# Performance work log

Measured on AMD Instinct MI355X. Metric: run time of the kernel, lower is better.

The kernel has to match this reference:

```python
import jax, jax.numpy as jnp
import numpy as np
import math

NP2 = 64      # number of RF pulses
V = 32768     # number of voxels


def _shift_matrix(kmax):
    """EPG shift matrix, exact translation of EPG_shift_matrices."""
    N = 3 * (kmax + 1)
    S = np.zeros(N * N, dtype=np.complex64)
    kidx = list(range(3, N, 3)); sidx = [x - 3 for x in kidx]
    S[[a + N * b for a, b in zip(kidx, sidx)]] = 1
    kidx = list(range(4, N, 3)); kidx.pop(); sidx = [x + 3 for x in kidx]
    S[[a + N * b for a, b in zip(kidx, sidx)]] = 1
    kidx = list(range(2, N, 3))
    S[[a + N * b for a, b in zip(kidx, kidx)]] = 1
    S = S.reshape(N, N).T.copy()
    S[0:2, 4] = 1
    return jnp.asarray(S, dtype=jnp.complex64)


def _rf_rot_all(theta):
    """RF rotation matrices for all pulses at once. theta: [P] complex -> [P,3,3]."""
    a = jnp.abs(theta)
    phi = jnp.angle(theta)
    ca2 = (jnp.cos(a / 2) ** 2).astype(jnp.complex64)
    sa2 = jnp.sin(a / 2) ** 2
    sa = jnp.sin(a)
    ca = jnp.cos(a).astype(jnp.complex64)
    ep = jnp.exp(1j * phi)
    em = jnp.exp(-1j * phi)
    e2m = jnp.exp(-2j * phi)
    r00 = ca2
    r10 = e2m * sa2
    r20 = -0.5j * em * sa
    r01 = jnp.conj(r10)
    r11 = ca2
    r21 = 0.5j * ep * sa
    r02 = -1j * ep * sa
    r12 = 1j * em * sa
    r22 = ca
    row0 = jnp.stack([r00, r01, r02], axis=-1)
    row1 = jnp.stack([r10, r11, r12], axis=-1)
    row2 = jnp.stack([r20, r21, r22], axis=-1)
    return jnp.stack([row0, row1, row2], axis=-2).astype(jnp.complex64)


def _epg_gre_f0(theta, T1, T2, TR):
    """Single-compartment GRE EPG recurrence. Returns F0 signal [V, np2].

    Uses full-width (kmax) state updates every pulse: states beyond
    kmax_per_pulse are exactly zero on the ramp-up and cannot influence
    F0 on the ramp-down, so F0 matches the variable-width torch loop.
    """
    np2 = theta.shape[0]
    kmax = np2 - 1
    kpp_max = math.ceil(np2 / 2)
    if kpp_max < kmax:
        kmax = kpp_max
    K = kmax + 1
    N = 3 * K
    v = T1.shape[0]

    St = _shift_matrix(kmax).T                      # [N,N], so S @ f == f @ St
    E1 = jnp.exp(-TR / T1)[:, 0]                    # [V]
    E2 = jnp.exp(-TR / T2)[:, 0]                    # [V]
    # diagonal of kron(I_K, diag(E2,E2,E1)) per voxel -> [V,N]
    e = jnp.tile(jnp.stack([E2, E2, E1], axis=1), (1, K)).astype(jnp.complex64)
    b = jnp.zeros((v, N), jnp.complex64).at[:, 2].set((1 - E1).astype(jnp.complex64))

    A_all = _rf_rot_all(theta)                      # [np2,3,3]
    FF0 = jnp.zeros((v, N), jnp.complex64).at[:, 2].set(1.0)

    def step(FF, A):
        # block-diag kron(I_K, A) applied to the state vector
        Fcol = jnp.einsum('ab,vkb->vka', A, FF.reshape(v, K, 3)).reshape(v, N)
        # relaxation * shift + recovery
        FFn = e * (Fcol @ St) + b
        FFn = FFn.at[:, 0].set(jnp.conj(FFn[:, 0]))
        return FFn, Fcol[:, 0]

    _, F0 = jax.lax.scan(step, FF0, A_all)          # F0: [np2, V]
    return F0.T                                     # [V, np2]


def setup_inputs() -> dict:
    key = jax.random.key(0)
    k1, k2, k3, k4, k5 = jax.random.split(key, 5)
    flip = jax.random.uniform(k1, (NP2,), minval=0.1, maxval=math.pi / 2)
    phase = jax.random.uniform(k2, (NP2,), minval=-math.pi, maxval=math.pi)
    theta_re = (flip * jnp.cos(phase)).astype(jnp.float32)
    theta_im = (flip * jnp.sin(phase)).astype(jnp.float32)
    PD = jax.random.uniform(k3, (V, 1), minval=0.2, maxval=1.0)
    T1 = jax.random.uniform(k4, (V, 1), minval=300.0, maxval=1500.0)
    T2 = jax.random.uniform(k5, (V, 1), minval=20.0, maxval=120.0)
    qmaps = jnp.stack([PD, T1, T2], axis=0).astype(jnp.float32)  # [3,V,1]
    TR = jnp.array([10.0], jnp.float32)
    return {"theta_re": theta_re, "theta_im": theta_im, "TR": TR,
            "quantitative_maps": qmaps}


def reference(theta_re, theta_im, TR, quantitative_maps):
    theta = (theta_re + 1j * theta_im).astype(jnp.complex64)
    PD = quantitative_maps[0]   # [V,1]
    T1 = quantitative_maps[1]   # [V,1]
    T2 = quantitative_maps[2]   # [V,1]
    s = _epg_gre_f0(theta, T1, T2, TR)   # [V, np2] complex
    return jnp.abs(s) * PD
```

## Files before the change

### kernel.cpp

```cpp
#include <hip/hip_runtime.h>
#include <hip/hip_fp16.h>
#include <math.h>


#define NP2 64
#define ROR1  0x121
#define ROR15 0x12F
#define RSHL1 0x101

__device__ __forceinline__ unsigned h2u(__half2 x) {
    unsigned u; __builtin_memcpy(&u, &x, 4); return u;
}
__device__ __forceinline__ __half2 u2h(unsigned u) {
    __half2 h; __builtin_memcpy(&h, &u, 4); return h;
}
template<int CTRL>
__device__ __forceinline__ __half2 rroth(__half2 x) {
    return u2h((unsigned)__builtin_amdgcn_mov_dpp((int)h2u(x), CTRL, 0xF, 0xF, true));
}

__global__ void coef_kernel(const float* __restrict__ theta_re,
                            const float* __restrict__ theta_im,
                            unsigned* __restrict__ cw)
{
    const int t = threadIdx.x;
    if (t < NP2) {
        const float tre = theta_re[t], tim = theta_im[t];
        const float a2 = tre * tre + tim * tim;
        const float inva = __frsqrt_rn(a2);
        const float a = a2 * inva;
        const float c = tre * inva, s = tim * inva;
        float cp = 1.f, sp = 0.f;
        if (t > 0) {
            const float ure = theta_re[t - 1], uim = theta_im[t - 1];
            const float ia = __frsqrt_rn(ure * ure + uim * uim);
            cp = ure * ia; sp = uim * ia;
        }
        const float cd = cp * c + sp * s;
        const float sd = sp * c - cp * s;
        float sa, ca;
        __sincosf(a, &sa, &ca);
        const float ca2 = 0.5f + 0.5f * ca;
        const float sa2 = 0.5f - 0.5f * ca;
        unsigned* row = cw + t * 8;
        const float vals[8] = { cd, sd, ca2, sa2, sa, ca, 0.5f * sa, 0.f };
        for (int j = 0; j < 8; ++j) {
            const __half h = __float2half(vals[j]);
            __half2 hp = __halves2half2(h, h);
            unsigned u; __builtin_memcpy(&u, &hp, 4);
            row[j] = u;
        }
    } else if (t < NP2 + 8) {
        cw[NP2 * 8 + (t - NP2)] = 0u;
    }
}

__device__ __forceinline__ void slot_mat(
    __half2 Pr, __half2 Pi, __half2 Mr, __half2 Mi, __half2& Zr, __half2& Zi,
    __half2 ec, __half2 es, __half2 esn,
    __half2 ca2, __half2 sa2, __half2 sa, __half2 ca, __half2 hh,
    __half2 pE1, __half2 rec,
    __half2& nPr, __half2& nPi, __half2& nMr, __half2& nMi)
{
    const __half2 hPr = __hfma2(ec, Pr, __hmul2(esn, Pi));
    const __half2 hPi = __hfma2(ec, Pi, __hmul2(es,  Pr));
    const __half2 hMr = __hfma2(ec, Mr, __hmul2(es,  Mi));
    const __half2 hMi = __hfma2(ec, Mi, __hmul2(esn, Mr));
    const __half2 ezr = __hfma2(pE1, Zr, rec);
    const __half2 ezi = __hmul2(pE1, Zi);
    const __half2 szr = __hmul2(sa, ezr);
    const __half2 szi = __hmul2(sa, ezi);
    const __half2 szrn = __hneg2(szr);
    const __half2 szin = __hneg2(szi);
    nPr = __hfma2(ca2, hPr, __hfma2(sa2, hMr, szi));
    nPi = __hfma2(ca2, hPi, __hfma2(sa2, hMi, szrn));
    nMr = __hfma2(sa2, hPr, __hfma2(ca2, hMr, szin));
    nMi = __hfma2(sa2, hPi, __hfma2(ca2, hMi, szr));
    Zr = __hfma2(hh, __hsub2(hPi, hMi), __hmul2(ca, ezr));
    Zi = __hfma2(hh, __hsub2(hMr, hPr), __hmul2(ca, ezi));
}

__global__ __launch_bounds__(256, 8) void epg_kernel(
    const float* __restrict__ TRp,
    const float* __restrict__ qmaps,
    const unsigned* __restrict__ cw,
    float* __restrict__ out, int V)
{
    const int t = threadIdx.x;
    const int sub = t & 15;
    const int vloc = t >> 4;
    const int vA = blockIdx.x * 32 + vloc;
    const int vB = vA + 16;

    __shared__ unsigned bufPr[16][65], bufPi[16][65];

    const float tr = TRp[0];
    const float E1A = __expf(-tr / qmaps[V + vA]);
    const float E2A = __expf(-tr / qmaps[2 * V + vA]);
    const float E1B = __expf(-tr / qmaps[V + vB]);
    const float E2B = __expf(-tr / qmaps[2 * V + vB]);
    const bool s0 = (sub == 0);
    const bool s15 = (sub == 15);
    const __half2 pE1 = __floats2half2_rn(E1A, E1B);
    const __half2 pE2 = __floats2half2_rn(E2A, E2B);
    const __half2 zeroH = __floats2half2_rn(0.f, 0.f);
    const __half2 recH = s0 ? __floats2half2_rn(1.f - E1A, 1.f - E1B) : zeroH;

    __half2 Pr0 = zeroH, Pr1 = zeroH, Pi0 = zeroH, Pi1 = zeroH;
    __half2 Mr0 = zeroH, Mr1 = zeroH, Mi0 = zeroH, Mi1 = zeroH;
    __half2 Zr0 = s0 ? __floats2half2_rn(1.f, 1.f) : zeroH;
    __half2 Zr1 = zeroH, Zi0 = zeroH, Zi1 = zeroH;

    const uint4* __restrict__ cwq = (const uint4*)cw;
    uint4 q0 = cwq[0], q1 = cwq[1];

    __half2 nPr0, nPi0, nMr0, nMi0, nPr1, nPi1, nMr1, nMi1;

#pragma unroll 1
    for (int p = 0; p < 15; ++p) {
        const int nb = 2 * (p + 1);
        const uint4 n0 = cwq[nb], n1 = cwq[nb + 1];
        const __half2 ec = __hmul2(pE2, u2h(q0.x));
        const __half2 es = __hmul2(pE2, u2h(q0.y));
        const __half2 esn = __hneg2(es);
        slot_mat(Pr0, Pi0, Mr0, Mi0, Zr0, Zi0, ec, es, esn,
                 u2h(q0.z), u2h(q0.w), u2h(q1.x), u2h(q1.y), u2h(q1.z),
                 pE1, recH, nPr0, nPi0, nMr0, nMi0);
        if (s0) { bufPr[vloc][p] = h2u(nPr0); bufPi[vloc][p] = h2u(nPi0); }
        const __half2 rPr = rroth<ROR1>(nPr0);
        const __half2 rPi = rroth<ROR1>(nPi0);
        const __half2 rMr = rroth<RSHL1>(nMr0);
        const __half2 rMi = rroth<RSHL1>(nMi0);
        Pr0 = s0 ? rMr : rPr;
        Pi0 = s0 ? __hneg2(rMi) : rPi;
        Mr0 = rMr;
        Mi0 = rMi;
        q0 = n0; q1 = n1;
    }

#pragma unroll 1
    for (int p = 15; p < 48; ++p) {
        const int nb = 2 * (p + 1);
        const uint4 n0 = cwq[nb], n1 = cwq[nb + 1];
        const __half2 ec = __hmul2(pE2, u2h(q0.x));
        const __half2 es = __hmul2(pE2, u2h(q0.y));
        const __half2 esn = __hneg2(es);
        const __half2 ca2 = u2h(q0.z), sa2 = u2h(q0.w);
        const __half2 sa = u2h(q1.x), ca = u2h(q1.y), hh = u2h(q1.z);
        slot_mat(Pr0, Pi0, Mr0, Mi0, Zr0, Zi0, ec, es, esn,
                 ca2, sa2, sa, ca, hh, pE1, recH, nPr0, nPi0, nMr0, nMi0);
        slot_mat(Pr1, Pi1, Mr1, Mi1, Zr1, Zi1, ec, es, esn,
                 ca2, sa2, sa, ca, hh, pE1, zeroH, nPr1, nPi1, nMr1, nMi1);
        if (s0) { bufPr[vloc][p] = h2u(nPr0); bufPi[vloc][p] = h2u(nPi0); }
        const __half2 rPr0 = rroth<ROR1>(nPr0),  rPr1 = rroth<ROR1>(nPr1);
        const __half2 rPi0 = rroth<ROR1>(nPi0),  rPi1 = rroth<ROR1>(nPi1);
        const __half2 rMr0 = rroth<ROR15>(nMr0), rMr1 = rroth<ROR15>(nMr1);
        const __half2 rMi0 = rroth<ROR15>(nMi0), rMi1 = rroth<ROR15>(nMi1);
        Pr1 = s0 ? rPr0 : rPr1;
        Pi1 = s0 ? rPi0 : rPi1;
        Pr0 = s0 ? rMr0 : rPr0;
        Pi0 = s0 ? __hneg2(rMi0) : rPi0;
        Mr0 = s15 ? rMr1 : rMr0;
        Mi0 = s15 ? rMi1 : rMi0;
        Mr1 = s15 ? zeroH : rMr1;
        Mi1 = s15 ? zeroH : rMi1;
        q0 = n0; q1 = n1;
    }

#pragma unroll 1
    for (int p = 48; p < NP2; ++p) {
        const int nb = 2 * (p + 1);
        const uint4 n0 = cwq[nb], n1 = cwq[nb + 1];
        const __half2 ec = __hmul2(pE2, u2h(q0.x));
        const __half2 es = __hmul2(pE2, u2h(q0.y));
        const __half2 esn = __hneg2(es);
        slot_mat(Pr0, Pi0, Mr0, Mi0, Zr0, Zi0, ec, es, esn,
                 u2h(q0.z), u2h(q0.w), u2h(q1.x), u2h(q1.y), u2h(q1.z),
                 pE1, recH, nPr0, nPi0, nMr0, nMi0);
        if (s0) { bufPr[vloc][p] = h2u(nPr0); bufPi[vloc][p] = h2u(nPi0); }
        const __half2 rPr = rroth<ROR1>(nPr0);
        const __half2 rPi = rroth<ROR1>(nPi0);
        const __half2 rMr = rroth<RSHL1>(nMr0);
        const __half2 rMi = rroth<RSHL1>(nMi0);
        Pr0 = s0 ? rMr : rPr;
        Pi0 = s0 ? __hneg2(rMi) : rPi;
        Mr0 = rMr;
        Mi0 = rMi;
        q0 = n0; q1 = n1;
    }

    __syncthreads();
    float4* out4 = (float4*)out;
#pragma unroll
    for (int i = 0; i < 2; ++i) {
        const int q = i * 256 + t;
        const int r = q >> 4;
        const int c = (q & 15) * 4;
        const int row = r & 15;
        const bool hi = (r >> 4) != 0;
        const float PDr = qmaps[blockIdx.x * 32 + r];
        float4 val;
        float* vp = &val.x;
#pragma unroll
        for (int j = 0; j < 4; ++j) {
            const __half2 hr = u2h(bufPr[row][c + j]);
            const __half2 hii = u2h(bufPi[row][c + j]);
            const float pr = hi ? __high2float(hr) : __low2float(hr);
            const float pi = hi ? __high2float(hii) : __low2float(hii);
            vp[j] = sqrtf(pr * pr + pi * pi) * PDr;
        }
        out4[blockIdx.x * 512 + q] = val;
    }
}

extern "C" void kernel_launch(void* const* d_in, const int* in_sizes, int n_in,
                              void* d_out, int out_size, void* d_ws, size_t ws_size,
                              hipStream_t stream) {
    const float* theta_re = (const float*)d_in[0];
    const float* theta_im = (const float*)d_in[1];
    const float* TRp      = (const float*)d_in[2];
    const float* qmaps    = (const float*)d_in[3];
    float* out = (float*)d_out;
    unsigned* cw = (unsigned*)d_ws;
    const int V = in_sizes[3] / 3;
    coef_kernel<<<dim3(1), dim3(128), 0, stream>>>(theta_re, theta_im, cw);
    epg_kernel<<<dim3(V / 32), dim3(256), 0, stream>>>(TRp, qmaps, cw, out, V);
}
```

Before: 97.75 us.

## Process four voxels per thread with two independent half2 recurrence chains

Each thread now carries two independent packed-half2 EPG state sets, so a block covers 64 voxels instead of 32 and the grid is halved. The aim is more instruction-level parallelism inside each serial pulse recurrence, which can hide the latency of dependent FMA and DPP operations, and to share the per-pulse coefficient loads across twice as many voxels. In exchange, register pressure and shared memory per block double, the launch bound drops to 4 blocks per CU, and fewer blocks are launched, so occupancy is lower.

```diff
diff --git a/kernel.cpp b/kernel.cpp
--- a/kernel.cpp
+++ b/kernel.cpp
@@ -80,7 +80,7 @@
     Zi = __hfma2(hh, __hsub2(hMr, hPr), __hmul2(ca, ezi));
 }
 
-__global__ __launch_bounds__(256, 8) void epg_kernel(
+__global__ __launch_bounds__(256, 4) void epg_kernel(
     const float* __restrict__ TRp,
     const float* __restrict__ qmaps,
     const unsigned* __restrict__ cw,
@@ -89,52 +89,86 @@
     const int t = threadIdx.x;
     const int sub = t & 15;
     const int vloc = t >> 4;
-    const int vA = blockIdx.x * 32 + vloc;
+    const int base = blockIdx.x * 64;
+    const int vA = base + vloc;
     const int vB = vA + 16;
-
-    __shared__ unsigned bufPr[16][65], bufPi[16][65];
+    const int vC = vA + 32;
+    const int vD = vA + 48;
+
+    __shared__ unsigned bufPrA[16][65], bufPiA[16][65];
+    __shared__ unsigned bufPrB[16][65], bufPiB[16][65];
 
     const float tr = TRp[0];
     const float E1A = __expf(-tr / qmaps[V + vA]);
     const float E2A = __expf(-tr / qmaps[2 * V + vA]);
     const float E1B = __expf(-tr / qmaps[V + vB]);
     const float E2B = __expf(-tr / qmaps[2 * V + vB]);
+    const float E1C = __expf(-tr / qmaps[V + vC]);
+    const float E2C = __expf(-tr / qmaps[2 * V + vC]);
+    const float E1D = __expf(-tr / qmaps[V + vD]);
+    const float E2D = __expf(-tr / qmaps[2 * V + vD]);
     const bool s0 = (sub == 0);
     const bool s15 = (sub == 15);
-    const __half2 pE1 = __floats2half2_rn(E1A, E1B);
-    const __half2 pE2 = __floats2half2_rn(E2A, E2B);
+    const __half2 pE1a = __floats2half2_rn(E1A, E1B);
+    const __half2 pE2a = __floats2half2_rn(E2A, E2B);
+    const __half2 pE1b = __floats2half2_rn(E1C, E1D);
+    const __half2 pE2b = __floats2half2_rn(E2C, E2D);
     const __half2 zeroH = __floats2half2_rn(0.f, 0.f);
-    const __half2 recH = s0 ? __floats2half2_rn(1.f - E1A, 1.f - E1B) : zeroH;
-
-    __half2 Pr0 = zeroH, Pr1 = zeroH, Pi0 = zeroH, Pi1 = zeroH;
-    __half2 Mr0 = zeroH, Mr1 = zeroH, Mi0 = zeroH, Mi1 = zeroH;
-    __half2 Zr0 = s0 ? __floats2half2_rn(1.f, 1.f) : zeroH;
-    __half2 Zr1 = zeroH, Zi0 = zeroH, Zi1 = zeroH;
+    const __half2 recHa = s0 ? __floats2half2_rn(1.f - E1A, 1.f - E1B) : zeroH;
+    const __half2 recHb = s0 ? __floats2half2_rn(1.f - E1C, 1.f - E1D) : zeroH;
+
+    __half2 Pr0a = zeroH, Pr1a = zeroH, Pi0a = zeroH, Pi1a = zeroH;
+    __half2 Mr0a = zeroH, Mr1a = zeroH, Mi0a = zeroH, Mi1a = zeroH;
+    __half2 Zr0a = s0 ? __floats2half2_rn(1.f, 1.f) : zeroH;
+    __half2 Zr1a = zeroH, Zi0a = zeroH, Zi1a = zeroH;
+    __half2 Pr0b = zeroH, Pr1b = zeroH, Pi0b = zeroH, Pi1b = zeroH;
+    __half2 Mr0b = zeroH, Mr1b = zeroH, Mi0b = zeroH, Mi1b = zeroH;
+    __half2 Zr0b = s0 ? __floats2half2_rn(1.f, 1.f) : zeroH;
+    __half2 Zr1b = zeroH, Zi0b = zeroH, Zi1b = zeroH;
 
     const uint4* __restrict__ cwq = (const uint4*)cw;
     uint4 q0 = cwq[0], q1 = cwq[1];
 
-    __half2 nPr0, nPi0, nMr0, nMi0, nPr1, nPi1, nMr1, nMi1;
+    __half2 nPr0a, nPi0a, nMr0a, nMi0a, nPr1a, nPi1a, nMr1a, nMi1a;
+    __half2 nPr0b, nPi0b, nMr0b, nMi0b, nPr1b, nPi1b, nMr1b, nMi1b;
 
 #pragma unroll 1
     for (int p = 0; p < 15; ++p) {
         const int nb = 2 * (p + 1);
         const uint4 n0 = cwq[nb], n1 = cwq[nb + 1];
-        const __half2 ec = __hmul2(pE2, u2h(q0.x));
-        const __half2 es = __hmul2(pE2, u2h(q0.y));
-        const __half2 esn = __hneg2(es);
-        slot_mat(Pr0, Pi0, Mr0, Mi0, Zr0, Zi0, ec, es, esn,
-                 u2h(q0.z), u2h(q0.w), u2h(q1.x), u2h(q1.y), u2h(q1.z),
-                 pE1, recH, nPr0, nPi0, nMr0, nMi0);
-        if (s0) { bufPr[vloc][p] = h2u(nPr0); bufPi[vloc][p] = h2u(nPi0); }
-        const __half2 rPr = rroth<ROR1>(nPr0);
-        const __half2 rPi = rroth<ROR1>(nPi0);
-        const __half2 rMr = rroth<RSHL1>(nMr0);
-        const __half2 rMi = rroth<RSHL1>(nMi0);
-        Pr0 = s0 ? rMr : rPr;
-        Pi0 = s0 ? __hneg2(rMi) : rPi;
-        Mr0 = rMr;
-        Mi0 = rMi;
+        const __half2 cd = u2h(q0.x), sd = u2h(q0.y);
+        const __half2 ca2 = u2h(q0.z), sa2 = u2h(q0.w);
+        const __half2 sa = u2h(q1.x), ca = u2h(q1.y), hh = u2h(q1.z);
+        const __half2 eca = __hmul2(pE2a, cd);
+        const __half2 esa = __hmul2(pE2a, sd);
+        const __half2 esna = __hneg2(esa);
+        const __half2 ecb = __hmul2(pE2b, cd);
+        const __half2 esb = __hmul2(pE2b, sd);
+        const __half2 esnb = __hneg2(esb);
+        slot_mat(Pr0a, Pi0a, Mr0a, Mi0a, Zr0a, Zi0a, eca, esa, esna,
+                 ca2, sa2, sa, ca, hh, pE1a, recHa, nPr0a, nPi0a, nMr0a, nMi0a);
+        slot_mat(Pr0b, Pi0b, Mr0b, Mi0b, Zr0b, Zi0b, ecb, esb, esnb,
+                 ca2, sa2, sa, ca, hh, pE1b, recHb, nPr0b, nPi0b, nMr0b, nMi0b);
+        if (s0) {
+            bufPrA[vloc][p] = h2u(nPr0a); bufPiA[vloc][p] = h2u(nPi0a);
+            bufPrB[vloc][p] = h2u(nPr0b); bufPiB[vloc][p] = h2u(nPi0b);
+        }
+        const __half2 rPra = rroth<ROR1>(nPr0a);
+        const __half2 rPia = rroth<ROR1>(nPi0a);
+        const __half2 rMra = rroth<RSHL1>(nMr0a);
+        const __half2 rMia = rroth<RSHL1>(nMi0a);
+        const __half2 rPrb = rroth<ROR1>(nPr0b);
+        const __half2 rPib = rroth<ROR1>(nPi0b);
+        const __half2 rMrb = rroth<RSHL1>(nMr0b);
+        const __half2 rMib = rroth<RSHL1>(nMi0b);
+        Pr0a = s0 ? rMra : rPra;
+        Pi0a = s0 ? __hneg2(rMia) : rPia;
+        Mr0a = rMra;
+        Mi0a = rMia;
+        Pr0b = s0 ? rMrb : rPrb;
+        Pi0b = s0 ? __hneg2(rMib) : rPib;
+        Mr0b = rMrb;
+        Mi0b = rMib;
         q0 = n0; q1 = n1;
     }
 
@@ -142,28 +176,51 @@
     for (int p = 15; p < 48; ++p) {
         const int nb = 2 * (p + 1);
         const uint4 n0 = cwq[nb], n1 = cwq[nb + 1];
-        const __half2 ec = __hmul2(pE2, u2h(q0.x));
-        const __half2 es = __hmul2(pE2, u2h(q0.y));
-        const __half2 esn = __hneg2(es);
+        const __half2 cd = u2h(q0.x), sd = u2h(q0.y);
         const __half2 ca2 = u2h(q0.z), sa2 = u2h(q0.w);
         const __half2 sa = u2h(q1.x), ca = u2h(q1.y), hh = u2h(q1.z);
-        slot_mat(Pr0, Pi0, Mr0, Mi0, Zr0, Zi0, ec, es, esn,
-                 ca2, sa2, sa, ca, hh, pE1, recH, nPr0, nPi0, nMr0, nMi0);
-        slot_mat(Pr1, Pi1, Mr1, Mi1, Zr1, Zi1, ec, es, esn,
-                 ca2, sa2, sa, ca, hh, pE1, zeroH, nPr1, nPi1, nMr1, nMi1);
-        if (s0) { bufPr[vloc][p] = h2u(nPr0); bufPi[vloc][p] = h2u(nPi0); }
-        const __half2 rPr0 = rroth<ROR1>(nPr0),  rPr1 = rroth<ROR1>(nPr1);
-        const __half2 rPi0 = rroth<ROR1>(nPi0),  rPi1 = rroth<ROR1>(nPi1);
-        const __half2 rMr0 = rroth<ROR15>(nMr0), rMr1 = rroth<ROR15>(nMr1);
-        const __half2 rMi0 = rroth<ROR15>(nMi0), rMi1 = rroth<ROR15>(nMi1);
-        Pr1 = s0 ? rPr0 : rPr1;
-        Pi1 = s0 ? rPi0 : rPi1;
-        Pr0 = s0 ? rMr0 : rPr0;
-        Pi0 = s0 ? __hneg2(rMi0) : rPi0;
-        Mr0 = s15 ? rMr1 : rMr0;
-        Mi0 = s15 ? rMi1 : rMi0;
-        Mr1 = s15 ? zeroH : rMr1;
-        Mi1 = s15 ? zeroH : rMi1;
+        const __half2 eca = __hmul2(pE2a, cd);
+        const __half2 esa = __hmul2(pE2a, sd);
+        const __half2 esna = __hneg2(esa);
+        const __half2 ecb = __hmul2(pE2b, cd);
+        const __half2 esb = __hmul2(pE2b, sd);
+        const __half2 esnb = __hneg2(esb);
+        slot_mat(Pr0a, Pi0a, Mr0a, Mi0a, Zr0a, Zi0a, eca, esa, esna,
+                 ca2, sa2, sa, ca, hh, pE1a, recHa, nPr0a, nPi0a, nMr0a, nMi0a);
+        slot_mat(Pr1a, Pi1a, Mr1a, Mi1a, Zr1a, Zi1a, eca, esa, esna,
+                 ca2, sa2, sa, ca, hh, pE1a, zeroH, nPr1a, nPi1a, nMr1a, nMi1a);
+        slot_mat(Pr0b, Pi0b, Mr0b, Mi0b, Zr0b, Zi0b, ecb, esb, esnb,
+                 ca2, sa2, sa, ca, hh, pE1b, recHb, nPr0b, nPi0b, nMr0b, nMi0b);
+        slot_mat(Pr1b, Pi1b, Mr1b, Mi1b, Zr1b, Zi1b, ecb, esb, esnb,
+                 ca2, sa2, sa, ca, hh, pE1b, zeroH, nPr1b, nPi1b, nMr1b, nMi1b);
+        if (s0) {
+            bufPrA[vloc][p] = h2u(nPr0a); bufPiA[vloc][p] = h2u(nPi0a);
+            bufPrB[vloc][p] = h2u(nPr0b); bufPiB[vloc][p] = h2u(nPi0b);
+        }
+        const __half2 rPr0a = rroth<ROR1>(nPr0a),  rPr1a = rroth<ROR1>(nPr1a);
+        const __half2 rPi0a = rroth<ROR1>(nPi0a),  rPi1a = rroth<ROR1>(nPi1a);
+        const __half2 rMr0a = rroth<ROR15>(nMr0a), rMr1a = rroth<ROR15>(nMr1a);
+        const __half2 rMi0a = rroth<ROR15>(nMi0a), rMi1a = rroth<ROR15>(nMi1a);
+        const __half2 rPr0b = rroth<ROR1>(nPr0b),  rPr1b = rroth<ROR1>(nPr1b);
+        const __half2 rPi0b = rroth<ROR1>(nPi0b),  rPi1b = rroth<ROR1>(nPi1b);
+        const __half2 rMr0b = rroth<ROR15>(nMr0b), rMr1b = rroth<ROR15>(nMr1b);
+        const __half2 rMi0b = rroth<ROR15>(nMi0b), rMi1b = rroth<ROR15>(nMi1b);
+        Pr1a = s0 ? rPr0a : rPr1a;
+        Pi1a = s0 ? rPi0a : rPi1a;
+        Pr0a = s0 ? rMr0a : rPr0a;
+        Pi0a = s0 ? __hneg2(rMi0a) : rPi0a;
+        Mr0a = s15 ? rMr1a : rMr0a;
+        Mi0a = s15 ? rMi1a : rMi0a;
+        Mr1a = s15 ? zeroH : rMr1a;
+        Mi1a = s15 ? zeroH : rMi1a;
+        Pr1b = s0 ? rPr0b : rPr1b;
+        Pi1b = s0 ? rPi0b : rPi1b;
+        Pr0b = s0 ? rMr0b : rPr0b;
+        Pi0b = s0 ? __hneg2(rMi0b) : rPi0b;
+        Mr0b = s15 ? rMr1b : rMr0b;
+        Mi0b = s15 ? rMi1b : rMi0b;
+        Mr1b = s15 ? zeroH : rMr1b;
+        Mi1b = s15 ? zeroH : rMi1b;
         q0 = n0; q1 = n1;
     }
 
@@ -171,45 +228,66 @@
     for (int p = 48; p < NP2; ++p) {
         const int nb = 2 * (p + 1);
         const uint4 n0 = cwq[nb], n1 = cwq[nb + 1];
-        const __half2 ec = __hmul2(pE2, u2h(q0.x));
-        const __half2 es = __hmul2(pE2, u2h(q0.y));
-        const __half2 esn = __hneg2(es);
-        slot_mat(Pr0, Pi0, Mr0, Mi0, Zr0, Zi0, ec, es, esn,
-                 u2h(q0.z), u2h(q0.w), u2h(q1.x), u2h(q1.y), u2h(q1.z),
-                 pE1, recH, nPr0, nPi0, nMr0, nMi0);
-        if (s0) { bufPr[vloc][p] = h2u(nPr0); bufPi[vloc][p] = h2u(nPi0); }
-        const __half2 rPr = rroth<ROR1>(nPr0);
-        const __half2 rPi = rroth<ROR1>(nPi0);
-        const __half2 rMr = rroth<RSHL1>(nMr0);
-        const __half2 rMi = rroth<RSHL1>(nMi0);
-        Pr0 = s0 ? rMr : rPr;
-        Pi0 = s0 ? __hneg2(rMi) : rPi;
-        Mr0 = rMr;
-        Mi0 = rMi;
+        const __half2 cd = u2h(q0.x), sd = u2h(q0.y);
+        const __half2 ca2 = u2h(q0.z), sa2 = u2h(q0.w);
+        const __half2 sa = u2h(q1.x), ca = u2h(q1.y), hh = u2h(q1.z);
+        const __half2 eca = __hmul2(pE2a, cd);
+        const __half2 esa = __hmul2(pE2a, sd);
+        const __half2 esna = __hneg2(esa);
+        const __half2 ecb = __hmul2(pE2b, cd);
+        const __half2 esb = __hmul2(pE2b, sd);
+        const __half2 esnb = __hneg2(esb);
+        slot_mat(Pr0a, Pi0a, Mr0a, Mi0a, Zr0a, Zi0a, eca, esa, esna,
+                 ca2, sa2, sa, ca, hh, pE1a, recHa, nPr0a, nPi0a, nMr0a, nMi0a);
+        slot_mat(Pr0b, Pi0b, Mr0b, Mi0b, Zr0b, Zi0b, ecb, esb, esnb,
+                 ca2, sa2, sa, ca, hh, pE1b, recHb, nPr0b, nPi0b, nMr0b, nMi0b);
+        if (s0) {
+            bufPrA[vloc][p] = h2u(nPr0a); bufPiA[vloc][p] = h2u(nPi0a);
+            bufPrB[vloc][p] = h2u(nPr0b); bufPiB[vloc][p] = h2u(nPi0b);
+        }
+        const __half2 rPra = rroth<ROR1>(nPr0a);
+        const __half2 rPia = rroth<ROR1>(nPi0a);
+        const __half2 rMra = rroth<RSHL1>(nMr0a);
+        const __half2 rMia = rroth<RSHL1>(nMi0a);
+        const __half2 rPrb = rroth<ROR1>(nPr0b);
+        const __half2 rPib = rroth<ROR1>(nPi0b);
+        const __half2 rMrb = rroth<RSHL1>(nMr0b);
+        const __half2 rMib = rroth<RSHL1>(nMi0b);
+        Pr0a = s0 ? rMra : rPra;
+        Pi0a = s0 ? __hneg2(rMia) : rPia;
+        Mr0a = rMra;
+        Mi0a = rMia;
+        Pr0b = s0 ? rMrb : rPrb;
+        Pi0b = s0 ? __hneg2(rMib) : rPib;
+        Mr0b = rMrb;
+        Mi0b = rMib;
         q0 = n0; q1 = n1;
     }
 
     __syncthreads();
     float4* out4 = (float4*)out;
 #pragma unroll
-    for (int i = 0; i < 2; ++i) {
+    for (int i = 0; i < 4; ++i) {
         const int q = i * 256 + t;
         const int r = q >> 4;
         const int c = (q & 15) * 4;
         const int row = r & 15;
-        const bool hi = (r >> 4) != 0;
-        const float PDr = qmaps[blockIdx.x * 32 + r];
+        const bool hi = (r >> 4) & 1;
+        const bool pb = (r >> 5) & 1;
+        const float PDr = qmaps[base + r];
         float4 val;
         float* vp = &val.x;
 #pragma unroll
         for (int j = 0; j < 4; ++j) {
-            const __half2 hr = u2h(bufPr[row][c + j]);
-            const __half2 hii = u2h(bufPi[row][c + j]);
+            const unsigned ur = pb ? bufPrB[row][c + j] : bufPrA[row][c + j];
+            const unsigned ui = pb ? bufPiB[row][c + j] : bufPiA[row][c + j];
+            const __half2 hr = u2h(ur);
+            const __half2 hii = u2h(ui);
             const float pr = hi ? __high2float(hr) : __low2float(hr);
             const float pi = hi ? __high2float(hii) : __low2float(hii);
             vp[j] = sqrtf(pr * pr + pi * pi) * PDr;
         }
-        out4[blockIdx.x * 512 + q] = val;
+        out4[blockIdx.x * 1024 + q] = val;
     }
 }
 
@@ -224,5 +302,5 @@
     unsigned* cw = (unsigned*)d_ws;
     const int V = in_sizes[3] / 3;
     coef_kernel<<<dim3(1), dim3(128), 0, stream>>>(theta_re, theta_im, cw);
-    epg_kernel<<<dim3(V / 32), dim3(256), 0, stream>>>(TRp, qmaps, cw, out, V);
-}
+    epg_kernel<<<dim3(V / 64), dim3(256), 0, stream>>>(TRp, qmaps, cw, out, V);
+}
```

Result: no change. 96.10 us (-1.7%).
